# Performance work log

Measured on AMD Instinct MI355X. Metric: run time of the kernel, lower is better.

Reference implementation:

```python
import jax, jax.numpy as jnp
import numpy as np

P = 1024 * 1024  # pixels (coordinate rows) the CPPN is evaluated on
N_IN, H, N_OUT = 12, 32, 3

# Activation library (CPPN-style): 0=identity, 1=tanh, 2=sigmoid, 3=sin, 4=gaussian
_ACTS = [
    lambda x: x,
    jnp.tanh,
    jax.nn.sigmoid,
    jnp.sin,
    lambda x: jnp.exp(-0.5 * x * x),
]

def _apply_acts(pre, ids):
    # pre: [P, n], ids: [n] int per-node activation id (Node.set_activation)
    out = pre
    for k, f in enumerate(_ACTS):
        if k == 0:
            out = f(pre)
        else:
            out = jnp.where(ids == k, f(pre), out)
    return out


def setup_inputs() -> dict:
    key = jax.random.key(0)
    ks = jax.random.split(key, 12)
    def w(k, shape, fan_in):
        return jax.random.normal(k, shape, jnp.float32) / np.sqrt(fan_in)
    inputs = jax.random.normal(ks[0], (P, N_IN), jnp.float32)
    return {
        "inputs": inputs,
        "bias_in": jnp.zeros((N_IN,), jnp.float32),
        "W1": w(ks[1], (N_IN, H), N_IN),
        "b1": 0.1 * jax.random.normal(ks[2], (H,), jnp.float32),
        "act1": jax.random.randint(ks[3], (H,), 0, 5, jnp.int32),
        "W2": w(ks[4], (H, H), H),
        "b2": 0.1 * jax.random.normal(ks[5], (H,), jnp.float32),
        "act2": jax.random.randint(ks[6], (H,), 0, 5, jnp.int32),
        "W3": w(ks[7], (H, H), H),
        "b3": 0.1 * jax.random.normal(ks[8], (H,), jnp.float32),
        "act3": jax.random.randint(ks[9], (H,), 0, 5, jnp.int32),
        "Wout": w(ks[10], (H, N_OUT), H),
        "bout": 0.1 * jax.random.normal(ks[11], (N_OUT,), jnp.float32),
    }


def reference(inputs, bias_in, W1, b1, act1, W2, b2, act2, W3, b3, act3, Wout, bout):
    # Input nodes: Node.forward = identity(x + bias)
    h0 = inputs + bias_in
    # Each hidden layer: per-edge scalar multiply + sum (== matvec since fully
    # connected between consecutive layers), then per-node bias + activation.
    h1 = _apply_acts(h0 @ W1 + b1, act1)
    h2 = _apply_acts(h1 @ W2 + b2, act2)
    h3 = _apply_acts(h2 @ W3 + b3, act3)
    # Output nodes use config.output_activation = tanh
    return jnp.tanh(h3 @ Wout + bout)
```

## Files before the change

kernel.cpp:

```cpp
#include <hip/hip_runtime.h>
#include <hip/hip_bf16.h>


#define BLK 256
#define NT 16

constexpr int NIN = 12, HID = 32, NOUT = 3;

typedef __attribute__((ext_vector_type(8))) short short8v;
typedef __attribute__((ext_vector_type(4))) float f32x4;

__device__ __forceinline__ unsigned short f2bf(float f) {
    unsigned u = __builtin_bit_cast(unsigned, f);
    u += 0x7FFFu + ((u >> 16) & 1u);
    return (unsigned short)(u >> 16);
}

__device__ __forceinline__ float tanh_fast(float x) {
    float e = __expf(2.0f * x);
    return 1.0f - 2.0f * __builtin_amdgcn_rcpf(e + 1.0f);
}

__device__ __forceinline__ float act_apply(float x, int id) {
    float e_in = (id == 1) ? (x + x) : ((id == 4) ? (-0.5f * x * x) : -x);
    float e = __expf(e_in);
    float r = __builtin_amdgcn_rcpf(e + 1.0f);
    float res = x;
    res = (id == 1) ? fmaf(-2.0f, r, 1.0f) : res;
    res = (id == 2) ? r : res;
    res = (id == 3) ? __sinf(x) : res;
    res = (id == 4) ? e : res;
    return res;
}

__global__ void __launch_bounds__(BLK, 4) cppn_mfma(
    const float* __restrict__ xin, const float* __restrict__ bin,
    const float* __restrict__ W1, const float* __restrict__ b1, const int* __restrict__ a1,
    const float* __restrict__ W2, const float* __restrict__ b2, const int* __restrict__ a2,
    const float* __restrict__ W3, const float* __restrict__ b3, const int* __restrict__ a3,
    const float* __restrict__ Wo, const float* __restrict__ bo,
    float* __restrict__ out, int Ppix) {
    const int tid = threadIdx.x;
    const int lane = tid & 63;
    const int wid = tid >> 6;
    const int q = lane >> 4;
    const int l15 = lane & 15;

    short8v w1f[2], w2f[2], w3f[2], wof;
#pragma unroll
    for (int t = 0; t < 2; ++t) {
#pragma unroll
        for (int j = 0; j < 8; ++j) {
            int k1 = 8 * q + j;
            float v1 = (k1 < NIN) ? W1[k1 * HID + 16 * t + l15]
                     : (k1 == NIN ? b1[16 * t + l15] : 0.0f);
            w1f[t][j] = (short)f2bf(v1);
            int k2 = 16 * (j >> 2) + 4 * q + (j & 3);
            w2f[t][j] = (short)f2bf(W2[k2 * HID + 16 * t + l15]);
            w3f[t][j] = (short)f2bf(W3[k2 * HID + 16 * t + l15]);
        }
    }
#pragma unroll
    for (int j = 0; j < 8; ++j) {
        int k2 = 16 * (j >> 2) + 4 * q + (j & 3);
        wof[j] = (l15 < NOUT) ? (short)f2bf(Wo[k2 * NOUT + l15]) : (short)0;
    }

    f32x4 b2f[2], b3f[2], bof;
#pragma unroll
    for (int t = 0; t < 2; ++t) {
#pragma unroll
        for (int r = 0; r < 4; ++r) {
            b2f[t][r] = b2[16 * t + 4 * q + r];
            b3f[t][r] = b3[16 * t + 4 * q + r];
        }
    }
#pragma unroll
    for (int r = 0; r < 4; ++r) bof[r] = (q == 0 && r < NOUT) ? bo[r] : 0.0f;

    int a1v[8], a2v[8], a3v[8];
#pragma unroll
    for (int e = 0; e < 8; ++e) {
        int j = 16 * (e >> 2) + 4 * q + (e & 3);
        a1v[e] = a1[j]; a2v[e] = a2[j]; a3v[e] = a3[j];
    }

    float binv[8];
#pragma unroll
    for (int j = 0; j < 8; ++j) {
        int k = 8 * q + j;
        binv[j] = (k < NIN) ? bin[k] : 0.0f;
    }

    const long long waveIdx = (long long)blockIdx.x * (BLK / 64) + wid;
    const long long px0 = waveIdx * (NT * 16);
    const f32x4 z = {0.0f, 0.0f, 0.0f, 0.0f};

    for (int it = 0; it < NT; ++it) {
        const long long px = px0 + it * 16 + l15;
        const bool ok = (px < Ppix);

        short8v b0f = {0, 0, 0, 0, 0, 0, 0, 0};
        if (q == 0) {
            f32x4 xa = ok ? *reinterpret_cast<const f32x4*>(xin + px * NIN)     : z;
            f32x4 xb = ok ? *reinterpret_cast<const f32x4*>(xin + px * NIN + 4) : z;
#pragma unroll
            for (int j = 0; j < 4; ++j) b0f[j]     = (short)f2bf(xa[j] + binv[j]);
#pragma unroll
            for (int j = 0; j < 4; ++j) b0f[4 + j] = (short)f2bf(xb[j] + binv[4 + j]);
        } else if (q == 1) {
            f32x4 xc = ok ? *reinterpret_cast<const f32x4*>(xin + px * NIN + 8) : z;
#pragma unroll
            for (int j = 0; j < 4; ++j) b0f[j] = (short)f2bf(xc[j] + binv[j]);
            b0f[4] = (short)0x3F80;
        }

        f32x4 p0 = __builtin_amdgcn_mfma_f32_16x16x32_bf16(w1f[0], b0f, z, 0, 0, 0);
        f32x4 p1 = __builtin_amdgcn_mfma_f32_16x16x32_bf16(w1f[1], b0f, z, 0, 0, 0);
        short8v hb;
#pragma unroll
        for (int r = 0; r < 4; ++r) hb[r]     = (short)f2bf(act_apply(p0[r], a1v[r]));
#pragma unroll
        for (int r = 0; r < 4; ++r) hb[4 + r] = (short)f2bf(act_apply(p1[r], a1v[4 + r]));

        p0 = __builtin_amdgcn_mfma_f32_16x16x32_bf16(w2f[0], hb, b2f[0], 0, 0, 0);
        p1 = __builtin_amdgcn_mfma_f32_16x16x32_bf16(w2f[1], hb, b2f[1], 0, 0, 0);
#pragma unroll
        for (int r = 0; r < 4; ++r) hb[r]     = (short)f2bf(act_apply(p0[r], a2v[r]));
#pragma unroll
        for (int r = 0; r < 4; ++r) hb[4 + r] = (short)f2bf(act_apply(p1[r], a2v[4 + r]));

        p0 = __builtin_amdgcn_mfma_f32_16x16x32_bf16(w3f[0], hb, b3f[0], 0, 0, 0);
        p1 = __builtin_amdgcn_mfma_f32_16x16x32_bf16(w3f[1], hb, b3f[1], 0, 0, 0);
#pragma unroll
        for (int r = 0; r < 4; ++r) hb[r]     = (short)f2bf(act_apply(p0[r], a3v[r]));
#pragma unroll
        for (int r = 0; r < 4; ++r) hb[4 + r] = (short)f2bf(act_apply(p1[r], a3v[4 + r]));

        f32x4 o = __builtin_amdgcn_mfma_f32_16x16x32_bf16(wof, hb, bof, 0, 0, 0);
        if (q == 0 && ok) {
            out[px * 3 + 0] = tanh_fast(o[0]);
            out[px * 3 + 1] = tanh_fast(o[1]);
            out[px * 3 + 2] = tanh_fast(o[2]);
        }
    }
}

extern "C" void kernel_launch(void* const* d_in, const int* in_sizes, int n_in,
                              void* d_out, int out_size, void* d_ws, size_t ws_size,
                              hipStream_t stream) {
    (void)n_in; (void)out_size; (void)d_ws; (void)ws_size;
    const float* xin = (const float*)d_in[0];
    const float* bin = (const float*)d_in[1];
    const float* W1  = (const float*)d_in[2];
    const float* b1  = (const float*)d_in[3];
    const int*   a1  = (const int*)  d_in[4];
    const float* W2  = (const float*)d_in[5];
    const float* b2  = (const float*)d_in[6];
    const int*   a2  = (const int*)  d_in[7];
    const float* W3  = (const float*)d_in[8];
    const float* b3  = (const float*)d_in[9];
    const int*   a3  = (const int*)  d_in[10];
    const float* Wo  = (const float*)d_in[11];
    const float* bo  = (const float*)d_in[12];
    float* out = (float*)d_out;

    const int Ppix = in_sizes[0] / NIN;
    const int pxPerBlock = (BLK / 64) * NT * 16;
    const int grid = (Ppix + pxPerBlock - 1) / pxPerBlock;
    hipLaunchKernelGGL(cppn_mfma, dim3(grid), dim3(BLK), 0, stream,
                       xin, bin, W1, b1, a1, W2, b2, a2, W3, b3, a3, Wo, bo,
                       out, Ppix);
}
```

Measured before the change: 202.2 us.

## Permute hidden nodes by activation id so MFMA row groups get uniform activations

Builds a per-layer permutation of the hidden neurons, computed with ballots and popcounts, that sorts nodes by activation type. Weights, biases and activation ids are loaded in permuted order, so the network output is unchanged. When the four rows a lane holds share one activation, that lane runs a single scalar-uniform activation instead of the branchless all-activation select. The change also adds packed bf16 conversion, a guard-free template for full blocks with a separate tail launch, and a non-unrolled pixel loop. The setup cost rises, and the speedup depends on how often the sorted node groups line up, which rests on the activation distribution.

Result: faster. 189.2 us (-6.4%).

```diff
diff --git a/kernel.cpp b/kernel.cpp
--- a/kernel.cpp
+++ b/kernel.cpp
@@ -9,6 +9,7 @@
 
 typedef __attribute__((ext_vector_type(8))) short short8v;
 typedef __attribute__((ext_vector_type(4))) float f32x4;
+typedef __attribute__((ext_vector_type(4))) unsigned uint4v;
 
 __device__ __forceinline__ unsigned short f2bf(float f) {
     unsigned u = __builtin_bit_cast(unsigned, f);
@@ -16,12 +17,26 @@
     return (unsigned short)(u >> 16);
 }
 
+__device__ __forceinline__ unsigned pk2(float lo, float hi) {
+    __hip_bfloat162 h = __float22bfloat162_rn(make_float2(lo, hi));
+    unsigned r; __builtin_memcpy(&r, &h, 4);
+    return r;
+}
+
 __device__ __forceinline__ float tanh_fast(float x) {
     float e = __expf(2.0f * x);
     return 1.0f - 2.0f * __builtin_amdgcn_rcpf(e + 1.0f);
 }
 
-__device__ __forceinline__ float act_apply(float x, int id) {
+__device__ __forceinline__ float act_uniform(float x, int sid) {
+    if (sid == 0) return x;
+    if (sid == 1) return tanh_fast(x);
+    if (sid == 2) return __builtin_amdgcn_rcpf(1.0f + __expf(-x));
+    if (sid == 3) return __sinf(x);
+    return __expf(-0.5f * x * x);
+}
+
+__device__ __forceinline__ float act_lane(float x, int id) {
     float e_in = (id == 1) ? (x + x) : ((id == 4) ? (-0.5f * x * x) : -x);
     float e = __expf(e_in);
     float r = __builtin_amdgcn_rcpf(e + 1.0f);
@@ -33,57 +48,147 @@
     return res;
 }
 
+template <bool GUARD>
 __global__ void __launch_bounds__(BLK, 4) cppn_mfma(
     const float* __restrict__ xin, const float* __restrict__ bin,
     const float* __restrict__ W1, const float* __restrict__ b1, const int* __restrict__ a1,
     const float* __restrict__ W2, const float* __restrict__ b2, const int* __restrict__ a2,
     const float* __restrict__ W3, const float* __restrict__ b3, const int* __restrict__ a3,
     const float* __restrict__ Wo, const float* __restrict__ bo,
-    float* __restrict__ out, int Ppix) {
+    float* __restrict__ out, int Ppix, int pxBase) {
     const int tid = threadIdx.x;
     const int lane = tid & 63;
     const int wid = tid >> 6;
     const int q = lane >> 4;
     const int l15 = lane & 15;
-
+    const int n = lane & 31;
+
+    auto build_perm = [&](const int* __restrict__ a) -> int {
+        int myid = a[n];
+        unsigned m0 = (unsigned)__ballot(myid == 0);
+        unsigned m1 = (unsigned)__ballot(myid == 1);
+        unsigned m2 = (unsigned)__ballot(myid == 2);
+        unsigned m3 = (unsigned)__ballot(myid == 3);
+        unsigned m4 = (unsigned)__ballot(myid == 4);
+        int c0 = __popc(m0), c1 = __popc(m1), c2 = __popc(m2), c3 = __popc(m3);
+        int pre = 0;
+        pre = (myid == 1) ? c0 : pre;
+        pre = (myid == 2) ? c0 + c1 : pre;
+        pre = (myid == 3) ? c0 + c1 + c2 : pre;
+        pre = (myid == 4) ? c0 + c1 + c2 + c3 : pre;
+        unsigned mm = m0;
+        mm = (myid == 1) ? m1 : mm;
+        mm = (myid == 2) ? m2 : mm;
+        mm = (myid == 3) ? m3 : mm;
+        mm = (myid == 4) ? m4 : mm;
+        unsigned lt = (1u << n) - 1u;
+        int pos = pre + __popc(mm & lt);
+        int npr = ((pos >> 4) << 4) + ((pos & 3) << 2) + ((pos >> 2) & 3);
+        int perm = __builtin_amdgcn_ds_permute(npr << 2, n);
+        return perm & 31;
+    };
+    const int perm1 = build_perm(a1);
+    const int perm2 = build_perm(a2);
+    const int perm3 = build_perm(a3);
+
+    auto pat = [&](int permv, int idx) -> int {
+        return __builtin_amdgcn_ds_bpermute(idx << 2, permv) & 31;
+    };
+
+    int o1[2], o2[2], o3[2];
+#pragma unroll
+    for (int t = 0; t < 2; ++t) {
+        o1[t] = pat(perm1, 16 * t + l15);
+        o2[t] = pat(perm2, 16 * t + l15);
+        o3[t] = pat(perm3, 16 * t + l15);
+    }
+    int i2v[8], i3v[8], iov[8];
+#pragma unroll
+    for (int j = 0; j < 8; ++j) {
+        int kk = 16 * (j >> 2) + 4 * q + (j & 3);
+        i2v[j] = pat(perm1, kk);
+        i3v[j] = pat(perm2, kk);
+        iov[j] = pat(perm3, kk);
+    }
     short8v w1f[2], w2f[2], w3f[2], wof;
 #pragma unroll
     for (int t = 0; t < 2; ++t) {
 #pragma unroll
         for (int j = 0; j < 8; ++j) {
             int k1 = 8 * q + j;
-            float v1 = (k1 < NIN) ? W1[k1 * HID + 16 * t + l15]
-                     : (k1 == NIN ? b1[16 * t + l15] : 0.0f);
+            float v1 = (k1 < NIN) ? W1[k1 * HID + o1[t]]
+                     : (k1 == NIN ? b1[o1[t]] : 0.0f);
             w1f[t][j] = (short)f2bf(v1);
-            int k2 = 16 * (j >> 2) + 4 * q + (j & 3);
-            w2f[t][j] = (short)f2bf(W2[k2 * HID + 16 * t + l15]);
-            w3f[t][j] = (short)f2bf(W3[k2 * HID + 16 * t + l15]);
-        }
-    }
-#pragma unroll
-    for (int j = 0; j < 8; ++j) {
-        int k2 = 16 * (j >> 2) + 4 * q + (j & 3);
-        wof[j] = (l15 < NOUT) ? (short)f2bf(Wo[k2 * NOUT + l15]) : (short)0;
-    }
+            w2f[t][j] = (short)f2bf(W2[i2v[j] * HID + o2[t]]);
+            w3f[t][j] = (short)f2bf(W3[i3v[j] * HID + o3[t]]);
+        }
+    }
+#pragma unroll
+    for (int j = 0; j < 8; ++j)
+        wof[j] = (l15 < NOUT) ? (short)f2bf(Wo[iov[j] * NOUT + l15]) : (short)0;
 
     f32x4 b2f[2], b3f[2], bof;
-#pragma unroll
-    for (int t = 0; t < 2; ++t) {
-#pragma unroll
-        for (int r = 0; r < 4; ++r) {
-            b2f[t][r] = b2[16 * t + 4 * q + r];
-            b3f[t][r] = b3[16 * t + 4 * q + r];
-        }
+    unsigned av1 = 0, av2 = 0, av3 = 0;
+#pragma unroll
+    for (int e = 0; e < 8; ++e) {
+        int t = e >> 2, r = e & 3;
+        int idx = 16 * t + 4 * q + r;
+        int p1i = pat(perm1, idx), p2i = pat(perm2, idx), p3i = pat(perm3, idx);
+        b2f[t][r] = b2[p2i];
+        b3f[t][r] = b3[p3i];
+        av1 |= (unsigned)(a1[p1i] & 15) << (4 * e);
+        av2 |= (unsigned)(a2[p2i] & 15) << (4 * e);
+        av3 |= (unsigned)(a3[p3i] & 15) << (4 * e);
     }
 #pragma unroll
     for (int r = 0; r < 4; ++r) bof[r] = (q == 0 && r < NOUT) ? bo[r] : 0.0f;
 
-    int a1v[8], a2v[8], a3v[8];
+    int idn1 = a1[perm1], idn2 = a2[perm2], idn3 = a3[perm3];
+    unsigned sidw1 = 0, sidw2 = 0, sidw3 = 0, prw1 = 0, prw2 = 0, prw3 = 0;
 #pragma unroll
     for (int e = 0; e < 8; ++e) {
-        int j = 16 * (e >> 2) + 4 * q + (e & 3);
-        a1v[e] = a1[j]; a2v[e] = a2[j]; a3v[e] = a3[j];
-    }
+        int g = 16 * (e >> 2) + (e & 3);
+        {
+            int s0 = __builtin_amdgcn_readlane(idn1, g);
+            int s1 = __builtin_amdgcn_readlane(idn1, g + 4);
+            int s2 = __builtin_amdgcn_readlane(idn1, g + 8);
+            int s3 = __builtin_amdgcn_readlane(idn1, g + 12);
+            sidw1 |= (unsigned)(s0 & 15) << (4 * e);
+            prw1 |= (unsigned)((s0 == s1) & (s0 == s2) & (s0 == s3)) << e;
+        }
+        {
+            int s0 = __builtin_amdgcn_readlane(idn2, g);
+            int s1 = __builtin_amdgcn_readlane(idn2, g + 4);
+            int s2 = __builtin_amdgcn_readlane(idn2, g + 8);
+            int s3 = __builtin_amdgcn_readlane(idn2, g + 12);
+            sidw2 |= (unsigned)(s0 & 15) << (4 * e);
+            prw2 |= (unsigned)((s0 == s1) & (s0 == s2) & (s0 == s3)) << e;
+        }
+        {
+            int s0 = __builtin_amdgcn_readlane(idn3, g);
+            int s1 = __builtin_amdgcn_readlane(idn3, g + 4);
+            int s2 = __builtin_amdgcn_readlane(idn3, g + 8);
+            int s3 = __builtin_amdgcn_readlane(idn3, g + 12);
+            sidw3 |= (unsigned)(s0 & 15) << (4 * e);
+            prw3 |= (unsigned)((s0 == s1) & (s0 == s2) & (s0 == s3)) << e;
+        }
+    }
+
+    auto actpack = [&](f32x4 p0, f32x4 p1, unsigned sidw, unsigned prw,
+                       unsigned av) -> uint4v {
+        float h[8];
+#pragma unroll
+        for (int e = 0; e < 8; ++e) {
+            float x = (e < 4) ? p0[e] : p1[e - 4];
+            int sid = (int)((sidw >> (4 * e)) & 15u);
+            if ((prw >> e) & 1u) h[e] = act_uniform(x, sid);
+            else                 h[e] = act_lane(x, (int)((av >> (4 * e)) & 15u));
+        }
+        uint4v w;
+        w[0] = pk2(h[0], h[1]); w[1] = pk2(h[2], h[3]);
+        w[2] = pk2(h[4], h[5]); w[3] = pk2(h[6], h[7]);
+        return w;
+    };
 
     float binv[8];
 #pragma unroll
@@ -92,56 +197,56 @@
         binv[j] = (k < NIN) ? bin[k] : 0.0f;
     }
 
-    const long long waveIdx = (long long)blockIdx.x * (BLK / 64) + wid;
-    const long long px0 = waveIdx * (NT * 16);
+    const long long wIdx = (long long)blockIdx.x * (BLK / 64) + wid;
+    const long long px0 = (long long)pxBase + wIdx * (NT * 16);
+    const float* __restrict__ xbase = xin + px0 * NIN;
+    float* __restrict__ obase = out + px0 * 3;
     const f32x4 z = {0.0f, 0.0f, 0.0f, 0.0f};
 
+#pragma unroll 1
     for (int it = 0; it < NT; ++it) {
-        const long long px = px0 + it * 16 + l15;
-        const bool ok = (px < Ppix);
-
-        short8v b0f = {0, 0, 0, 0, 0, 0, 0, 0};
+        const int po = it * 16 + l15;
+        const bool ok = !GUARD || (px0 + po < (long long)Ppix);
+
+        uint4v b0w = {0, 0, 0, 0};
         if (q == 0) {
-            f32x4 xa = ok ? *reinterpret_cast<const f32x4*>(xin + px * NIN)     : z;
-            f32x4 xb = ok ? *reinterpret_cast<const f32x4*>(xin + px * NIN + 4) : z;
-#pragma unroll
-            for (int j = 0; j < 4; ++j) b0f[j]     = (short)f2bf(xa[j] + binv[j]);
-#pragma unroll
-            for (int j = 0; j < 4; ++j) b0f[4 + j] = (short)f2bf(xb[j] + binv[4 + j]);
+            if (ok) {
+                const float4* ip = reinterpret_cast<const float4*>(xbase + po * NIN);
+                float4 xa = ip[0], xb = ip[1];
+                b0w[0] = pk2(xa.x + binv[0], xa.y + binv[1]);
+                b0w[1] = pk2(xa.z + binv[2], xa.w + binv[3]);
+                b0w[2] = pk2(xb.x + binv[4], xb.y + binv[5]);
+                b0w[3] = pk2(xb.z + binv[6], xb.w + binv[7]);
+            }
         } else if (q == 1) {
-            f32x4 xc = ok ? *reinterpret_cast<const f32x4*>(xin + px * NIN + 8) : z;
-#pragma unroll
-            for (int j = 0; j < 4; ++j) b0f[j] = (short)f2bf(xc[j] + binv[j]);
-            b0f[4] = (short)0x3F80;
-        }
-
-        f32x4 p0 = __builtin_amdgcn_mfma_f32_16x16x32_bf16(w1f[0], b0f, z, 0, 0, 0);
-        f32x4 p1 = __builtin_amdgcn_mfma_f32_16x16x32_bf16(w1f[1], b0f, z, 0, 0, 0);
-        short8v hb;
-#pragma unroll
-        for (int r = 0; r < 4; ++r) hb[r]     = (short)f2bf(act_apply(p0[r], a1v[r]));
-#pragma unroll
-        for (int r = 0; r < 4; ++r) hb[4 + r] = (short)f2bf(act_apply(p1[r], a1v[4 + r]));
-
+            if (ok) {
+                float4 xc = reinterpret_cast<const float4*>(xbase + po * NIN)[2];
+                b0w[0] = pk2(xc.x + binv[0], xc.y + binv[1]);
+                b0w[1] = pk2(xc.z + binv[2], xc.w + binv[3]);
+            }
+            b0w[2] = 0x3F80u;
+        }
+
+        short8v hb = __builtin_bit_cast(short8v, b0w);
+        f32x4 p0 = __builtin_amdgcn_mfma_f32_16x16x32_bf16(w1f[0], hb, z, 0, 0, 0);
+        f32x4 p1 = __builtin_amdgcn_mfma_f32_16x16x32_bf16(w1f[1], hb, z, 0, 0, 0);
+
+        hb = __builtin_bit_cast(short8v, actpack(p0, p1, sidw1, prw1, av1));
         p0 = __builtin_amdgcn_mfma_f32_16x16x32_bf16(w2f[0], hb, b2f[0], 0, 0, 0);
         p1 = __builtin_amdgcn_mfma_f32_16x16x32_bf16(w2f[1], hb, b2f[1], 0, 0, 0);
-#pragma unroll
-        for (int r = 0; r < 4; ++r) hb[r]     = (short)f2bf(act_apply(p0[r], a2v[r]));
-#pragma unroll
-        for (int r = 0; r < 4; ++r) hb[4 + r] = (short)f2bf(act_apply(p1[r], a2v[4 + r]));
-
+
+        hb = __builtin_bit_cast(short8v, actpack(p0, p1, sidw2, prw2, av2));
         p0 = __builtin_amdgcn_mfma_f32_16x16x32_bf16(w3f[0], hb, b3f[0], 0, 0, 0);
         p1 = __builtin_amdgcn_mfma_f32_16x16x32_bf16(w3f[1], hb, b3f[1], 0, 0, 0);
-#pragma unroll
-        for (int r = 0; r < 4; ++r) hb[r]     = (short)f2bf(act_apply(p0[r], a3v[r]));
-#pragma unroll
-        for (int r = 0; r < 4; ++r) hb[4 + r] = (short)f2bf(act_apply(p1[r], a3v[4 + r]));
-
-        f32x4 o = __builtin_amdgcn_mfma_f32_16x16x32_bf16(wof, hb, bof, 0, 0, 0);
+
+        hb = __builtin_bit_cast(short8v, actpack(p0, p1, sidw3, prw3, av3));
+        f32x4 o4 = __builtin_amdgcn_mfma_f32_16x16x32_bf16(wof, hb, bof, 0, 0, 0);
+
         if (q == 0 && ok) {
-            out[px * 3 + 0] = tanh_fast(o[0]);
-            out[px * 3 + 1] = tanh_fast(o[1]);
-            out[px * 3 + 2] = tanh_fast(o[2]);
+            float* op = obase + po * 3;
+            op[0] = tanh_fast(o4[0]);
+            op[1] = tanh_fast(o4[1]);
+            op[2] = tanh_fast(o4[2]);
         }
     }
 }
@@ -167,8 +272,14 @@
 
     const int Ppix = in_sizes[0] / NIN;
     const int pxPerBlock = (BLK / 64) * NT * 16;
-    const int grid = (Ppix + pxPerBlock - 1) / pxPerBlock;
-    hipLaunchKernelGGL(cppn_mfma, dim3(grid), dim3(BLK), 0, stream,
-                       xin, bin, W1, b1, a1, W2, b2, a2, W3, b3, a3, Wo, bo,
-                       out, Ppix);
-}
+    const int fullBlocks = Ppix / pxPerBlock;
+    const int rem = Ppix - fullBlocks * pxPerBlock;
+    if (fullBlocks > 0)
+        hipLaunchKernelGGL((cppn_mfma<false>), dim3(fullBlocks), dim3(BLK), 0, stream,
+                           xin, bin, W1, b1, a1, W2, b2, a2, W3, b3, a3, Wo, bo,
+                           out, Ppix, 0);
+    if (rem > 0)
+        hipLaunchKernelGGL((cppn_mfma<true>), dim3(1), dim3(BLK), 0, stream,
+                           xin, bin, W1, b1, a1, W2, b2, a2, W3, b3, a3, Wo, bo,
+                           out, Ppix, fullBlocks * pxPerBlock);
+}
```
